# Optimization experiments

Hardware: AMD Instinct MI355X
Metric: run time of the kernel (lower is better)

The kernel has to match this reference:

```python
import jax, jax.numpy as jnp
import numpy as np

N, D, C, O = 65536, 256, 1024, 64

def setup_inputs() -> dict:
    key = jax.random.key(0)
    k1, k2, k3, k4 = jax.random.split(key, 4)
    x = jax.random.normal(k1, (N, D), dtype=jnp.float32)
    centers = jax.random.normal(k2, (C, D), dtype=jnp.float32)
    sigma = jnp.ones((C,), dtype=jnp.float32)
    # nn.Linear(C, O): weight [O, C], bias [O]
    bound = 1.0 / np.sqrt(C)
    W = jax.random.uniform(k3, (O, C), minval=-bound, maxval=bound, dtype=jnp.float32)
    b = jax.random.uniform(k4, (O,), minval=-bound, maxval=bound, dtype=jnp.float32)
    return {"x": x, "centers": centers, "sigma": sigma, "W": W, "b": b}

def reference(x, centers, sigma, W, b):
    # dist_sq[n,c] = ||x_n - c_c||^2, via GEMM identity (same math as sum((x-c)**2))
    x_sq = jnp.sum(x * x, axis=-1, keepdims=True)              # [N,1]
    c_sq = jnp.sum(centers * centers, axis=-1)                 # [C]
    cross = jnp.einsum('nd,cd->nc', x, centers)                # [N,C]
    dist_sq = x_sq - 2.0 * cross + c_sq[None, :]               # [N,C]
    rbf = jnp.exp(-dist_sq / (2.0 * sigma ** 2 + 1e-8))        # [N,C]
    out = jnp.einsum('nc,oc->no', rbf, W) + b                  # [N,O]
    return out
```

## Files before the change

### kernel.cpp

```cpp
#include <hip/hip_runtime.h>
#include <stdint.h>

#define NROWS 65536
#define DIM   256
#define NC    1024
#define NO    64

#define BN    128
#define WROWS 32
#define BC    64
#define NTILE (NC / BC)

using bf16x8 = __bf16 __attribute__((ext_vector_type(8)));
using f32x4  = float __attribute__((ext_vector_type(4)));
using u16x4  = unsigned short __attribute__((ext_vector_type(4)));
using u32x2  = unsigned int __attribute__((ext_vector_type(2)));

#define MFMA16(a, b, c) __builtin_amdgcn_mfma_f32_16x16x32_bf16((a), (b), (c), 0, 0, 0)

__device__ inline unsigned short bf16_bits(float f) {
    __bf16 h = (__bf16)f;
    return __builtin_bit_cast(unsigned short, h);
}

__global__ __launch_bounds__(256) void prep(const float* __restrict__ cent,
                                            const float* __restrict__ sigma,
                                            const float* __restrict__ w,
                                            unsigned short* __restrict__ cbf,
                                            float* __restrict__ a2,
                                            float* __restrict__ aal,
                                            float* __restrict__ acs,
                                            unsigned short* __restrict__ wbf) {
    const int bid = blockIdx.x;
    if (bid < 256) {
        const int wid = threadIdx.x >> 6, lane = threadIdx.x & 63;
        const int c = bid * 4 + wid;
        float4 v = ((const float4*)cent)[(size_t)c * 64 + lane];
        u16x4 o;
        o[0] = bf16_bits(v.x); o[1] = bf16_bits(v.y);
        o[2] = bf16_bits(v.z); o[3] = bf16_bits(v.w);
        const int t = c >> 6, crow = c & 63, kc = lane >> 1;
        *(u16x4*)((char*)cbf + t * 32768 + (kc * 64 + crow) * 16 + (lane & 1) * 8) = o;
        float ss = v.x * v.x + v.y * v.y + v.z * v.z + v.w * v.w;
        #pragma unroll
        for (int off = 32; off; off >>= 1) ss += __shfl_down(ss, off);
        if (lane == 0) {
            float s = sigma[c];
            float al = 1.0f / (2.0f * s * s + 1e-8f);
            a2[c] = 2.0f * al;
            aal[c] = al;
            acs[c] = al * ss;
        }
    } else {
        const int o = bid - 256;
        float4 v = ((const float4*)w)[(size_t)o * 256 + threadIdx.x];
        u16x4 u;
        u[0] = bf16_bits(v.x); u[1] = bf16_bits(v.y);
        u[2] = bf16_bits(v.z); u[3] = bf16_bits(v.w);
        *(u16x4*)(wbf + (size_t)o * NC + threadIdx.x * 4) = u;
    }
}

__global__ __launch_bounds__(256, 2) void rbf_main(
    const float* __restrict__ x,
    const __bf16* __restrict__ cbf, const float* __restrict__ a2,
    const float* __restrict__ aal, const float* __restrict__ acs,
    const __bf16* __restrict__ wbf,
    const float* __restrict__ bias, float* __restrict__ out) {

    __shared__ __bf16 cent_lds[2][BC * DIM];
    __shared__ __bf16 rbf_lds[4][WROWS * BC];

    const int tid  = threadIdx.x;
    const int wid  = tid >> 6;
    const int lane = tid & 63;
    const int l15  = lane & 15;
    const int hi   = lane >> 4;

    const int rowbase = blockIdx.x * BN + wid * WROWS;

    auto stage = [&](int buf, int t) {
        const char* src = (const char*)cbf + (size_t)t * 32768 + (size_t)(wid * 64 + lane) * 16;
        char* dstb = (char*)&cent_lds[buf][0] + (wid * 64) * 16;
        #pragma unroll
        for (int i = 0; i < 8; ++i) {
            __builtin_amdgcn_global_load_lds(
                (const __attribute__((address_space(1))) uint32_t*)(src + i * 4096),
                (__attribute__((address_space(3))) uint32_t*)(dstb + i * 4096), 16, 0, 0);
        }
    };

    stage(0, 0);

    bf16x8 xf[2][8];
    float xsqv[2];
    #pragma unroll
    for (int nf = 0; nf < 2; ++nf) {
        const float* xr = x + (size_t)(rowbase + nf * 16 + l15) * DIM;
        float ss = 0.f;
        #pragma unroll
        for (int ks = 0; ks < 8; ++ks) {
            float4 a = *(const float4*)(xr + ks * 32 + hi * 8);
            float4 b = *(const float4*)(xr + ks * 32 + hi * 8 + 4);
            bf16x8 f;
            f[0] = (__bf16)a.x; f[1] = (__bf16)a.y; f[2] = (__bf16)a.z; f[3] = (__bf16)a.w;
            f[4] = (__bf16)b.x; f[5] = (__bf16)b.y; f[6] = (__bf16)b.z; f[7] = (__bf16)b.w;
            xf[nf][ks] = f;
            ss += a.x * a.x + a.y * a.y + a.z * a.z + a.w * a.w;
            ss += b.x * b.x + b.y * b.y + b.z * b.z + b.w * b.w;
        }
        ss += __shfl_xor(ss, 16);
        ss += __shfl_xor(ss, 32);
        xsqv[nf] = ss;
    }

    float bo[4];
    #pragma unroll
    for (int of = 0; of < 4; ++of) bo[of] = bias[of * 16 + l15];

    f32x4 oacc[2][4];
    #pragma unroll
    for (int nf = 0; nf < 2; ++nf)
        #pragma unroll
        for (int of = 0; of < 4; ++of) {
            f32x4 z = {0.f, 0.f, 0.f, 0.f};
            oacc[nf][of] = z;
        }

    asm volatile("s_waitcnt vmcnt(0)" ::: "memory");
    __syncthreads();

    int cur = 0;
    #pragma unroll 1
    for (int t = 0; t < NTILE; ++t) {
        if (t + 1 < NTILE) stage(cur ^ 1, t + 1);

        const char* cb = (const char*)&cent_lds[cur][0];
        f32x4 st[4][2];
        #pragma unroll
        for (int c4 = 0; c4 < 4; ++c4)
            #pragma unroll
            for (int nf = 0; nf < 2; ++nf) {
                f32x4 z = {0.f, 0.f, 0.f, 0.f};
                st[c4][nf] = z;
            }
        #pragma unroll
        for (int ks = 0; ks < 8; ++ks) {
            bf16x8 cf[4];
            #pragma unroll
            for (int c4 = 0; c4 < 4; ++c4)
                cf[c4] = *(const bf16x8*)(cb + ((ks * 4 + hi) * 64 + c4 * 16 + l15) * 16);
            #pragma unroll
            for (int c4 = 0; c4 < 4; ++c4)
                #pragma unroll
                for (int nf = 0; nf < 2; ++nf)
                    st[c4][nf] = MFMA16(cf[c4], xf[nf][ks], st[c4][nf]);
        }

        char* const rbase = (char*)&rbf_lds[wid][0];
        #pragma unroll
        for (int c4 = 0; c4 < 4; ++c4) {
            const int cg = t * BC + c4 * 16 + hi * 4;
            const f32x4 a24 = *(const f32x4*)(a2 + cg);
            const f32x4 al4 = *(const f32x4*)(aal + cg);
            const f32x4 ac4 = *(const f32x4*)(acs + cg);
            #pragma unroll
            for (int nf = 0; nf < 2; ++nf) {
                const f32x4 v = st[c4][nf];
                f32x4 t0;
                t0[0] = -al4[0] * xsqv[nf] - ac4[0];
                t0[1] = -al4[1] * xsqv[nf] - ac4[1];
                t0[2] = -al4[2] * xsqv[nf] - ac4[2];
                t0[3] = -al4[3] * xsqv[nf] - ac4[3];
                float p0 = __expf(a24[0] * v[0] + t0[0]);
                float p1 = __expf(a24[1] * v[1] + t0[1]);
                float p2 = __expf(a24[2] * v[2] + t0[2]);
                float p3 = __expf(a24[3] * v[3] + t0[3]);
                u32x2 wv;
                wv[0] = (unsigned)bf16_bits(p0) | ((unsigned)bf16_bits(p1) << 16);
                wv[1] = (unsigned)bf16_bits(p2) | ((unsigned)bf16_bits(p3) << 16);
                const int byte = ((c4 * 2 + (hi >> 1)) * 32 + nf * 16 + l15) * 16 + (hi & 1) * 8;
                *(u32x2*)(rbase + byte) = wv;
            }
        }

        #pragma unroll
        for (int cs = 0; cs < 2; ++cs) {
            bf16x8 pa[2];
            #pragma unroll
            for (int nf = 0; nf < 2; ++nf)
                pa[nf] = *(const bf16x8*)(rbase + ((cs * 4 + hi) * 32 + nf * 16 + l15) * 16);
            #pragma unroll
            for (int of = 0; of < 4; ++of) {
                const bf16x8 wb = *(const bf16x8*)(wbf + (size_t)(of * 16 + l15) * NC
                                                   + t * BC + cs * 32 + hi * 8);
                #pragma unroll
                for (int nf = 0; nf < 2; ++nf)
                    oacc[nf][of] = MFMA16(pa[nf], wb, oacc[nf][of]);
            }
        }

        asm volatile("s_waitcnt vmcnt(0)" ::: "memory");
        __syncthreads();
        cur ^= 1;
    }

    #pragma unroll
    for (int nf = 0; nf < 2; ++nf)
        #pragma unroll
        for (int of = 0; of < 4; ++of)
            #pragma unroll
            for (int r = 0; r < 4; ++r) {
                const int n = rowbase + nf * 16 + hi * 4 + r;
                out[(size_t)n * NO + of * 16 + l15] = oacc[nf][of][r] + bo[of];
            }
}

extern "C" void kernel_launch(void* const* d_in, const int* in_sizes, int n_in,
                              void* d_out, int out_size, void* d_ws, size_t ws_size,
                              hipStream_t stream) {
    const float* x     = (const float*)d_in[0];
    const float* cent  = (const float*)d_in[1];
    const float* sigma = (const float*)d_in[2];
    const float* W     = (const float*)d_in[3];
    const float* b     = (const float*)d_in[4];
    float* out = (float*)d_out;

    char* ws = (char*)d_ws;
    unsigned short* cbf  = (unsigned short*)(ws + 0);
    float*          a2p  = (float*)(ws + 524288);
    float*          aalp = (float*)(ws + 528384);
    float*          acsp = (float*)(ws + 532480);
    unsigned short* wbf  = (unsigned short*)(ws + 536576);

    prep<<<320, 256, 0, stream>>>(cent, sigma, W, cbf, a2p, aalp, acsp, wbf);
    rbf_main<<<NROWS / BN, 256, 0, stream>>>(
        x, (const __bf16*)cbf, a2p, aalp, acsp, (const __bf16*)wbf, b, out);
}
```

Measured before the change: 177.5 us.

## Halve rows per block, single-buffer center tiles, raise occupancy to four blocks

Each wave now handles 16 rows instead of 32 and each block 64 rows. The center-tile LDS staging drops from double to single buffering, with a load-wait-sync at the top of every tile. This cuts register and LDS footprint so the launch bound can request four blocks per CU, relying on occupancy to hide latency instead of software prefetch. In exchange, each staged center tile is reused by half as many rows, so total center and weight traffic from L2 doubles, and every tile load is now exposed inside its block.

```diff
diff --git a/kernel.cpp b/kernel.cpp
--- a/kernel.cpp
+++ b/kernel.cpp
@@ -6,8 +6,8 @@
 #define NC    1024
 #define NO    64
 
-#define BN    128
-#define WROWS 32
+#define BN    64
+#define WROWS 16
 #define BC    64
 #define NTILE (NC / BC)
 
@@ -61,14 +61,14 @@
     }
 }
 
-__global__ __launch_bounds__(256, 2) void rbf_main(
+__global__ __launch_bounds__(256, 4) void rbf_main(
     const float* __restrict__ x,
     const __bf16* __restrict__ cbf, const float* __restrict__ a2,
     const float* __restrict__ aal, const float* __restrict__ acs,
     const __bf16* __restrict__ wbf,
     const float* __restrict__ bias, float* __restrict__ out) {
 
-    __shared__ __bf16 cent_lds[2][BC * DIM];
+    __shared__ __bf16 cent_lds[BC * DIM];
     __shared__ __bf16 rbf_lds[4][WROWS * BC];
 
     const int tid  = threadIdx.x;
@@ -79,24 +79,10 @@
 
     const int rowbase = blockIdx.x * BN + wid * WROWS;
 
-    auto stage = [&](int buf, int t) {
-        const char* src = (const char*)cbf + (size_t)t * 32768 + (size_t)(wid * 64 + lane) * 16;
-        char* dstb = (char*)&cent_lds[buf][0] + (wid * 64) * 16;
-        #pragma unroll
-        for (int i = 0; i < 8; ++i) {
-            __builtin_amdgcn_global_load_lds(
-                (const __attribute__((address_space(1))) uint32_t*)(src + i * 4096),
-                (__attribute__((address_space(3))) uint32_t*)(dstb + i * 4096), 16, 0, 0);
-        }
-    };
-
-    stage(0, 0);
-
-    bf16x8 xf[2][8];
-    float xsqv[2];
-    #pragma unroll
-    for (int nf = 0; nf < 2; ++nf) {
-        const float* xr = x + (size_t)(rowbase + nf * 16 + l15) * DIM;
+    bf16x8 xf[8];
+    float xsqv;
+    {
+        const float* xr = x + (size_t)(rowbase + l15) * DIM;
         float ss = 0.f;
         #pragma unroll
         for (int ks = 0; ks < 8; ++ks) {
@@ -105,56 +91,58 @@
             bf16x8 f;
             f[0] = (__bf16)a.x; f[1] = (__bf16)a.y; f[2] = (__bf16)a.z; f[3] = (__bf16)a.w;
             f[4] = (__bf16)b.x; f[5] = (__bf16)b.y; f[6] = (__bf16)b.z; f[7] = (__bf16)b.w;
-            xf[nf][ks] = f;
+            xf[ks] = f;
             ss += a.x * a.x + a.y * a.y + a.z * a.z + a.w * a.w;
             ss += b.x * b.x + b.y * b.y + b.z * b.z + b.w * b.w;
         }
         ss += __shfl_xor(ss, 16);
         ss += __shfl_xor(ss, 32);
-        xsqv[nf] = ss;
+        xsqv = ss;
     }
 
     float bo[4];
     #pragma unroll
     for (int of = 0; of < 4; ++of) bo[of] = bias[of * 16 + l15];
 
-    f32x4 oacc[2][4];
+    f32x4 oacc[4];
     #pragma unroll
-    for (int nf = 0; nf < 2; ++nf)
-        #pragma unroll
-        for (int of = 0; of < 4; ++of) {
-            f32x4 z = {0.f, 0.f, 0.f, 0.f};
-            oacc[nf][of] = z;
-        }
-
-    asm volatile("s_waitcnt vmcnt(0)" ::: "memory");
-    __syncthreads();
-
-    int cur = 0;
+    for (int of = 0; of < 4; ++of) {
+        f32x4 z = {0.f, 0.f, 0.f, 0.f};
+        oacc[of] = z;
+    }
+
     #pragma unroll 1
     for (int t = 0; t < NTILE; ++t) {
-        if (t + 1 < NTILE) stage(cur ^ 1, t + 1);
-
-        const char* cb = (const char*)&cent_lds[cur][0];
-        f32x4 st[4][2];
-        #pragma unroll
-        for (int c4 = 0; c4 < 4; ++c4)
-            #pragma unroll
-            for (int nf = 0; nf < 2; ++nf) {
-                f32x4 z = {0.f, 0.f, 0.f, 0.f};
-                st[c4][nf] = z;
+        {
+            const char* src = (const char*)cbf + (size_t)t * 32768
+                              + (size_t)(wid * 64 + lane) * 16;
+            char* dstb = (char*)cent_lds + (wid * 64) * 16;
+            #pragma unroll
+            for (int i = 0; i < 8; ++i) {
+                __builtin_amdgcn_global_load_lds(
+                    (const __attribute__((address_space(1))) uint32_t*)(src + i * 4096),
+                    (__attribute__((address_space(3))) uint32_t*)(dstb + i * 4096), 16, 0, 0);
             }
+        }
+        asm volatile("s_waitcnt vmcnt(0)" ::: "memory");
+        __syncthreads();
+
+        f32x4 st[4];
+        #pragma unroll
+        for (int c4 = 0; c4 < 4; ++c4) {
+            f32x4 z = {0.f, 0.f, 0.f, 0.f};
+            st[c4] = z;
+        }
         #pragma unroll
         for (int ks = 0; ks < 8; ++ks) {
             bf16x8 cf[4];
             #pragma unroll
             for (int c4 = 0; c4 < 4; ++c4)
-                cf[c4] = *(const bf16x8*)(cb + ((ks * 4 + hi) * 64 + c4 * 16 + l15) * 16);
+                cf[c4] = *(const bf16x8*)((const char*)cent_lds
+                          + ((ks * 4 + hi) * 64 + c4 * 16 + l15) * 16);
             #pragma unroll
             for (int c4 = 0; c4 < 4; ++c4)
-                #pragma unroll
-                for (int nf = 0; nf < 2; ++nf)
-                    st[c4][nf] = MFMA16(cf[c4], xf[nf][ks], st[c4][nf]);
+                st[c4] = MFMA16(cf[c4], xf[ks], st[c4]);
         }
 
         char* const rbase = (char*)&rbf_lds[wid][0];
@@ -164,56 +152,39 @@
             const f32x4 a24 = *(const f32x4*)(a2 + cg);
             const f32x4 al4 = *(const f32x4*)(aal + cg);
             const f32x4 ac4 = *(const f32x4*)(acs + cg);
-            #pragma unroll
-            for (int nf = 0; nf < 2; ++nf) {
-                const f32x4 v = st[c4][nf];
-                f32x4 t0;
-                t0[0] = -al4[0] * xsqv[nf] - ac4[0];
-                t0[1] = -al4[1] * xsqv[nf] - ac4[1];
-                t0[2] = -al4[2] * xsqv[nf] - ac4[2];
-                t0[3] = -al4[3] * xsqv[nf] - ac4[3];
-                float p0 = __expf(a24[0] * v[0] + t0[0]);
-                float p1 = __expf(a24[1] * v[1] + t0[1]);
-                float p2 = __expf(a24[2] * v[2] + t0[2]);
-                float p3 = __expf(a24[3] * v[3] + t0[3]);
-                u32x2 wv;
-                wv[0] = (unsigned)bf16_bits(p0) | ((unsigned)bf16_bits(p1) << 16);
-                wv[1] = (unsigned)bf16_bits(p2) | ((unsigned)bf16_bits(p3) << 16);
-                const int byte = ((c4 * 2 + (hi >> 1)) * 32 + nf * 16 + l15) * 16 + (hi & 1) * 8;
-                *(u32x2*)(rbase + byte) = wv;
-            }
+            const f32x4 v = st[c4];
+            float p0 = __expf(a24[0] * v[0] - al4[0] * xsqv - ac4[0]);
+            float p1 = __expf(a24[1] * v[1] - al4[1] * xsqv - ac4[1]);
+            float p2 = __expf(a24[2] * v[2] - al4[2] * xsqv - ac4[2]);
+            float p3 = __expf(a24[3] * v[3] - al4[3] * xsqv - ac4[3]);
+            u32x2 wv;
+            wv[0] = (unsigned)bf16_bits(p0) | ((unsigned)bf16_bits(p1) << 16);
+            wv[1] = (unsigned)bf16_bits(p2) | ((unsigned)bf16_bits(p3) << 16);
+            const int byte = ((c4 * 2 + (hi >> 1)) * 16 + l15) * 16 + (hi & 1) * 8;
+            *(u32x2*)(rbase + byte) = wv;
         }
 
         #pragma unroll
         for (int cs = 0; cs < 2; ++cs) {
-            bf16x8 pa[2];
-            #pragma unroll
-            for (int nf = 0; nf < 2; ++nf)
-                pa[nf] = *(const bf16x8*)(rbase + ((cs * 4 + hi) * 32 + nf * 16 + l15) * 16);
+            const bf16x8 pa = *(const bf16x8*)(rbase + ((cs * 4 + hi) * 16 + l15) * 16);
             #pragma unroll
             for (int of = 0; of < 4; ++of) {
                 const bf16x8 wb = *(const bf16x8*)(wbf + (size_t)(of * 16 + l15) * NC
                                                    + t * BC + cs * 32 + hi * 8);
-                #pragma unroll
-                for (int nf = 0; nf < 2; ++nf)
-                    oacc[nf][of] = MFMA16(pa[nf], wb, oacc[nf][of]);
+                oacc[of] = MFMA16(pa, wb, oacc[of]);
             }
         }
 
-        asm volatile("s_waitcnt vmcnt(0)" ::: "memory");
         __syncthreads();
-        cur ^= 1;
     }
 
     #pragma unroll
-    for (int nf = 0; nf < 2; ++nf)
-        #pragma unroll
-        for (int of = 0; of < 4; ++of)
-            #pragma unroll
-            for (int r = 0; r < 4; ++r) {
-                const int n = rowbase + nf * 16 + hi * 4 + r;
-                out[(size_t)n * NO + of * 16 + l15] = oacc[nf][of][r] + bo[of];
-            }
+    for (int of = 0; of < 4; ++of)
+        #pragma unroll
+        for (int r = 0; r < 4; ++r) {
+            const int n = rowbase + hi * 4 + r;
+            out[(size_t)n * NO + of * 16 + l15] = oacc[of][r] + bo[of];
+        }
 }
 
 extern "C" void kernel_launch(void* const* d_in, const int* in_sizes, int n_in,
```

Result: slower. 200.8 us (+13.1%).

## Single-buffer larger center tiles and fold x_sq into exponent argument

Applied to the files above, without the earlier changes.

Doubles the center tile from 64 to 128 columns and replaces the double-buffered async staging with a single LDS buffer that is loaded and waited on at the start of each tile. Occupancy stays at two blocks per CU within the same LDS budget, and there are half as many loop iterations. The exponent is rewritten as a2*(cross - 0.5*x_sq) - acs, which drops the aal array and one multiply-add per element. In exchange, the global-to-LDS load no longer overlaps with compute, so each block stalls on every tile load unless the other resident block hides it.

```diff
diff --git a/kernel.cpp b/kernel.cpp
--- a/kernel.cpp
+++ b/kernel.cpp
@@ -8,7 +8,7 @@
 
 #define BN    128
 #define WROWS 32
-#define BC    64
+#define BC    128
 #define NTILE (NC / BC)
 
 using bf16x8 = __bf16 __attribute__((ext_vector_type(8)));
@@ -28,7 +28,6 @@
                                             const float* __restrict__ w,
                                             unsigned short* __restrict__ cbf,
                                             float* __restrict__ a2,
-                                            float* __restrict__ aal,
                                             float* __restrict__ acs,
                                             unsigned short* __restrict__ wbf) {
     const int bid = blockIdx.x;
@@ -39,8 +38,8 @@
         u16x4 o;
         o[0] = bf16_bits(v.x); o[1] = bf16_bits(v.y);
         o[2] = bf16_bits(v.z); o[3] = bf16_bits(v.w);
-        const int t = c >> 6, crow = c & 63, kc = lane >> 1;
-        *(u16x4*)((char*)cbf + t * 32768 + (kc * 64 + crow) * 16 + (lane & 1) * 8) = o;
+        const int t = c >> 7, crow = c & 127, kc = lane >> 1;
+        *(u16x4*)((char*)cbf + t * 65536 + (kc * 128 + crow) * 16 + (lane & 1) * 8) = o;
         float ss = v.x * v.x + v.y * v.y + v.z * v.z + v.w * v.w;
         #pragma unroll
         for (int off = 32; off; off >>= 1) ss += __shfl_down(ss, off);
@@ -48,7 +47,6 @@
             float s = sigma[c];
             float al = 1.0f / (2.0f * s * s + 1e-8f);
             a2[c] = 2.0f * al;
-            aal[c] = al;
             acs[c] = al * ss;
         }
     } else {
@@ -64,12 +62,11 @@
 __global__ __launch_bounds__(256, 2) void rbf_main(
     const float* __restrict__ x,
     const __bf16* __restrict__ cbf, const float* __restrict__ a2,
-    const float* __restrict__ aal, const float* __restrict__ acs,
-    const __bf16* __restrict__ wbf,
+    const float* __restrict__ acs, const __bf16* __restrict__ wbf,
     const float* __restrict__ bias, float* __restrict__ out) {
 
-    __shared__ __bf16 cent_lds[2][BC * DIM];
-    __shared__ __bf16 rbf_lds[4][WROWS * BC];
+    __shared__ __bf16 cent_lds[BC * DIM];
+    __shared__ __bf16 rbf_lds[4][WROWS * 64];
 
     const int tid  = threadIdx.x;
     const int wid  = tid >> 6;
@@ -79,21 +76,8 @@
 
     const int rowbase = blockIdx.x * BN + wid * WROWS;
 
-    auto stage = [&](int buf, int t) {
-        const char* src = (const char*)cbf + (size_t)t * 32768 + (size_t)(wid * 64 + lane) * 16;
-        char* dstb = (char*)&cent_lds[buf][0] + (wid * 64) * 16;
-        #pragma unroll
-        for (int i = 0; i < 8; ++i) {
-            __builtin_amdgcn_global_load_lds(
-                (const __attribute__((address_space(1))) uint32_t*)(src + i * 4096),
-                (__attribute__((address_space(3))) uint32_t*)(dstb + i * 4096), 16, 0, 0);
-        }
-    };
-
-    stage(0, 0);
-
     bf16x8 xf[2][8];
-    float xsqv[2];
+    float hxsq[2];
     #pragma unroll
     for (int nf = 0; nf < 2; ++nf) {
         const float* xr = x + (size_t)(rowbase + nf * 16 + l15) * DIM;
@@ -111,7 +95,7 @@
         }
         ss += __shfl_xor(ss, 16);
         ss += __shfl_xor(ss, 32);
-        xsqv[nf] = ss;
+        hxsq[nf] = 0.5f * ss;
     }
 
     float bo[4];
@@ -127,18 +111,26 @@
             oacc[nf][of] = z;
         }
 
-    asm volatile("s_waitcnt vmcnt(0)" ::: "memory");
-    __syncthreads();
-
-    int cur = 0;
     #pragma unroll 1
     for (int t = 0; t < NTILE; ++t) {
-        if (t + 1 < NTILE) stage(cur ^ 1, t + 1);
-
-        const char* cb = (const char*)&cent_lds[cur][0];
-        f32x4 st[4][2];
-        #pragma unroll
-        for (int c4 = 0; c4 < 4; ++c4)
+        __syncthreads();
+        {
+            const char* src = (const char*)cbf + (size_t)t * 65536
+                              + (size_t)(wid * 64 + lane) * 16;
+            char* dstb = (char*)cent_lds + (wid * 64) * 16;
+            #pragma unroll
+            for (int i = 0; i < 16; ++i) {
+                __builtin_amdgcn_global_load_lds(
+                    (const __attribute__((address_space(1))) uint32_t*)(src + i * 4096),
+                    (__attribute__((address_space(3))) uint32_t*)(dstb + i * 4096), 16, 0, 0);
+            }
+        }
+        asm volatile("s_waitcnt vmcnt(0)" ::: "memory");
+        __syncthreads();
+
+        f32x4 st[8][2];
+        #pragma unroll
+        for (int c4 = 0; c4 < 8; ++c4)
             #pragma unroll
             for (int nf = 0; nf < 2; ++nf) {
                 f32x4 z = {0.f, 0.f, 0.f, 0.f};
@@ -146,12 +138,13 @@
             }
         #pragma unroll
         for (int ks = 0; ks < 8; ++ks) {
-            bf16x8 cf[4];
-            #pragma unroll
-            for (int c4 = 0; c4 < 4; ++c4)
-                cf[c4] = *(const bf16x8*)(cb + ((ks * 4 + hi) * 64 + c4 * 16 + l15) * 16);
-            #pragma unroll
-            for (int c4 = 0; c4 < 4; ++c4)
+            bf16x8 cf[8];
+            #pragma unroll
+            for (int c4 = 0; c4 < 8; ++c4)
+                cf[c4] = *(const bf16x8*)((const char*)cent_lds
+                          + ((ks * 4 + hi) * 128 + c4 * 16 + l15) * 16);
+            #pragma unroll
+            for (int c4 = 0; c4 < 8; ++c4)
                 #pragma unroll
                 for (int nf = 0; nf < 2; ++nf)
                     st[c4][nf] = MFMA16(cf[c4], xf[nf][ks], st[c4][nf]);
@@ -159,50 +152,45 @@
 
         char* const rbase = (char*)&rbf_lds[wid][0];
         #pragma unroll
-        for (int c4 = 0; c4 < 4; ++c4) {
-            const int cg = t * BC + c4 * 16 + hi * 4;
-            const f32x4 a24 = *(const f32x4*)(a2 + cg);
-            const f32x4 al4 = *(const f32x4*)(aal + cg);
-            const f32x4 ac4 = *(const f32x4*)(acs + cg);
-            #pragma unroll
-            for (int nf = 0; nf < 2; ++nf) {
-                const f32x4 v = st[c4][nf];
-                f32x4 t0;
-                t0[0] = -al4[0] * xsqv[nf] - ac4[0];
-                t0[1] = -al4[1] * xsqv[nf] - ac4[1];
-                t0[2] = -al4[2] * xsqv[nf] - ac4[2];
-                t0[3] = -al4[3] * xsqv[nf] - ac4[3];
-                float p0 = __expf(a24[0] * v[0] + t0[0]);
-                float p1 = __expf(a24[1] * v[1] + t0[1]);
-                float p2 = __expf(a24[2] * v[2] + t0[2]);
-                float p3 = __expf(a24[3] * v[3] + t0[3]);
-                u32x2 wv;
-                wv[0] = (unsigned)bf16_bits(p0) | ((unsigned)bf16_bits(p1) << 16);
-                wv[1] = (unsigned)bf16_bits(p2) | ((unsigned)bf16_bits(p3) << 16);
-                const int byte = ((c4 * 2 + (hi >> 1)) * 32 + nf * 16 + l15) * 16 + (hi & 1) * 8;
-                *(u32x2*)(rbase + byte) = wv;
-            }
-        }
-
-        #pragma unroll
-        for (int cs = 0; cs < 2; ++cs) {
-            bf16x8 pa[2];
-            #pragma unroll
-            for (int nf = 0; nf < 2; ++nf)
-                pa[nf] = *(const bf16x8*)(rbase + ((cs * 4 + hi) * 32 + nf * 16 + l15) * 16);
-            #pragma unroll
-            for (int of = 0; of < 4; ++of) {
-                const bf16x8 wb = *(const bf16x8*)(wbf + (size_t)(of * 16 + l15) * NC
-                                                   + t * BC + cs * 32 + hi * 8);
+        for (int h = 0; h < 2; ++h) {
+            #pragma unroll
+            for (int c4h = 0; c4h < 4; ++c4h) {
+                const int c4 = h * 4 + c4h;
+                const int cg = t * BC + c4 * 16 + hi * 4;
+                const f32x4 a24 = *(const f32x4*)(a2 + cg);
+                const f32x4 ac4 = *(const f32x4*)(acs + cg);
+                #pragma unroll
+                for (int nf = 0; nf < 2; ++nf) {
+                    const f32x4 v = st[c4][nf];
+                    float p0 = __expf(a24[0] * (v[0] - hxsq[nf]) - ac4[0]);
+                    float p1 = __expf(a24[1] * (v[1] - hxsq[nf]) - ac4[1]);
+                    float p2 = __expf(a24[2] * (v[2] - hxsq[nf]) - ac4[2]);
+                    float p3 = __expf(a24[3] * (v[3] - hxsq[nf]) - ac4[3]);
+                    u32x2 wv;
+                    wv[0] = (unsigned)bf16_bits(p0) | ((unsigned)bf16_bits(p1) << 16);
+                    wv[1] = (unsigned)bf16_bits(p2) | ((unsigned)bf16_bits(p3) << 16);
+                    const int byte = ((c4h * 2 + (hi >> 1)) * 32 + nf * 16 + l15) * 16
+                                     + (hi & 1) * 8;
+                    *(u32x2*)(rbase + byte) = wv;
+                }
+            }
+            #pragma unroll
+            for (int cs = 0; cs < 2; ++cs) {
+                bf16x8 pa[2];
                 #pragma unroll
                 for (int nf = 0; nf < 2; ++nf)
-                    oacc[nf][of] = MFMA16(pa[nf], wb, oacc[nf][of]);
-            }
-        }
-
-        asm volatile("s_waitcnt vmcnt(0)" ::: "memory");
-        __syncthreads();
-        cur ^= 1;
+                    pa[nf] = *(const bf16x8*)(rbase
+                              + ((cs * 4 + hi) * 32 + nf * 16 + l15) * 16);
+                #pragma unroll
+                for (int of = 0; of < 4; ++of) {
+                    const bf16x8 wb = *(const bf16x8*)(wbf
+                        + (size_t)(of * 16 + l15) * NC + t * BC + h * 64 + cs * 32 + hi * 8);
+                    #pragma unroll
+                    for (int nf = 0; nf < 2; ++nf)
+                        oacc[nf][of] = MFMA16(pa[nf], wb, oacc[nf][of]);
+                }
+            }
+        }
     }
 
     #pragma unroll
@@ -229,11 +217,10 @@
     char* ws = (char*)d_ws;
     unsigned short* cbf  = (unsigned short*)(ws + 0);
     float*          a2p  = (float*)(ws + 524288);
-    float*          aalp = (float*)(ws + 528384);
-    float*          acsp = (float*)(ws + 532480);
-    unsigned short* wbf  = (unsigned short*)(ws + 536576);
-
-    prep<<<320, 256, 0, stream>>>(cent, sigma, W, cbf, a2p, aalp, acsp, wbf);
+    float*          acsp = (float*)(ws + 528384);
+    unsigned short* wbf  = (unsigned short*)(ws + 532480);
+
+    prep<<<320, 256, 0, stream>>>(cent, sigma, W, cbf, a2p, acsp, wbf);
     rbf_main<<<NROWS / BN, 256, 0, stream>>>(
-        x, (const __bf16*)cbf, a2p, aalp, acsp, (const __bf16*)wbf, b, out);
-}
+        x, (const __bf16*)cbf, a2p, acsp, (const __bf16*)wbf, b, out);
+}
```

New measurement: 169.6 us. -4.4%, faster.
